# Performance work log

Hardware: AMD Instinct MI355X
Metric: run time of the kernel (lower is better)

## Reference

```python
import jax, jax.numpy as jnp
import numpy as np

B, T, H, V = 32, 16, 768, 32000
EPS = 1e-5


def _conv(x, w, stride, pad):
    return jax.lax.conv_general_dilated(
        x, w, (stride, stride), [(pad, pad), (pad, pad)],
        dimension_numbers=('NCHW', 'OIHW', 'NCHW'))


def _bn(x, g, b, m, v):
    inv = g / jnp.sqrt(v + EPS)
    return x * inv[None, :, None, None] + (b - m * inv)[None, :, None, None]


def setup_inputs() -> dict:
    key = jax.random.key(0)
    ks = iter(jax.random.split(key, 48))

    def rn(shape, s=0.02):
        return s * jax.random.normal(next(ks), shape, jnp.float32)

    def bn_params(c):
        g = 1.0 + 0.1 * jax.random.normal(next(ks), (c,), jnp.float32)
        b = 0.1 * jax.random.normal(next(ks), (c,), jnp.float32)
        m = 0.1 * jax.random.normal(next(ks), (c,), jnp.float32)
        v = jax.random.uniform(next(ks), (c,), jnp.float32, 0.5, 1.5)
        return g, b, m, v

    inp = {}
    inp['images'] = jax.random.normal(next(ks), (B, 3, 224, 224), jnp.float32)
    inp['captions'] = jax.random.randint(next(ks), (B, T), 0, V)

    inp['conv1_w'] = rn((64, 3, 7, 7))
    inp['bn1_g'], inp['bn1_b'], inp['bn1_m'], inp['bn1_v'] = bn_params(64)
    inp['conv2_w'] = rn((128, 64, 3, 3))
    inp['bn2_g'], inp['bn2_b'], inp['bn2_m'], inp['bn2_v'] = bn_params(128)
    inp['conv3_w'] = rn((256, 128, 3, 3))
    inp['bn3_g'], inp['bn3_b'], inp['bn3_m'], inp['bn3_v'] = bn_params(256)
    inp['conv4_w'] = rn((H, 256, 3, 3))
    inp['bn4_g'], inp['bn4_b'], inp['bn4_m'], inp['bn4_v'] = bn_params(H)

    emb = rn((V, H), 1.0)
    inp['emb_table'] = emb.at[0].set(0.0)  # padding_idx=0 row is zero
    inp['attn_w'] = rn((H, H))             # attn_proj (no bias)
    inp['w_ih'] = rn((4 * H, 2 * H))       # LSTM input weights (i,f,g,o)
    inp['w_hh'] = rn((4 * H, H))
    inp['b_ih'] = rn((4 * H,))
    inp['b_hh'] = rn((4 * H,))
    inp['fc_w'] = rn((V, H))
    inp['fc_b'] = rn((V,))
    return inp


def _forward(images, captions, conv1_w, bn1_g, bn1_b, bn1_m, bn1_v,
             conv2_w, bn2_g, bn2_b, bn2_m, bn2_v,
             conv3_w, bn3_g, bn3_b, bn3_m, bn3_v,
             conv4_w, bn4_g, bn4_b, bn4_m, bn4_v,
             emb_table, attn_w, w_ih, w_hh, b_ih, b_hh, fc_w, fc_b):
    # ---- ResNetEncoder ----
    x = jax.nn.relu(_bn(_conv(images, conv1_w, 2, 3), bn1_g, bn1_b, bn1_m, bn1_v))
    x = jax.lax.reduce_window(x, -jnp.inf, jax.lax.max, (1, 1, 3, 3), (1, 1, 2, 2),
                              ((0, 0), (0, 0), (1, 1), (1, 1)))
    x = jax.nn.relu(_bn(_conv(x, conv2_w, 1, 1), bn2_g, bn2_b, bn2_m, bn2_v))
    x = jax.nn.relu(_bn(_conv(x, conv3_w, 2, 1), bn3_g, bn3_b, bn3_m, bn3_v))
    x = jax.nn.relu(_bn(_conv(x, conv4_w, 1, 1), bn4_g, bn4_b, bn4_m, bn4_v))
    b, c, hh, ww = x.shape
    memory = x.reshape(b, c, hh * ww).transpose(0, 2, 1)[:, :196, :]  # [B,196,H]

    # ---- LSTMAttnDecoder ----
    emb = emb_table[captions]  # [B,T,H]
    h0 = jnp.zeros((b, H), jnp.float32)
    c0 = jnp.zeros((b, H), jnp.float32)

    def step(carry, e_t):
        h, cst = carry
        q = h @ attn_w.T                                    # [B,H]
        scores = jnp.einsum('bh,bmh->bm', q, memory)        # [B,196]
        ctx = jnp.einsum('bm,bmh->bh', jax.nn.softmax(scores, axis=-1), memory)
        xin = jnp.concatenate([e_t, ctx], axis=-1)          # [B,2H]
        gates = xin @ w_ih.T + b_ih + h @ w_hh.T + b_hh     # [B,4H]
        i, f, g, o = jnp.split(gates, 4, axis=-1)
        c_new = jax.nn.sigmoid(f) * cst + jax.nn.sigmoid(i) * jnp.tanh(g)
        h_new = jax.nn.sigmoid(o) * jnp.tanh(c_new)
        logits = h_new @ fc_w.T + fc_b                      # [B,V]
        return (h_new, c_new), logits

    (hT, cT), logits = jax.lax.scan(step, (h0, c0), emb.transpose(1, 0, 2))
    logits = logits.transpose(1, 0, 2)  # [B,T,V]
    return logits, (hT[None], cT[None])


def reference(images, captions, conv1_w, bn1_g, bn1_b, bn1_m, bn1_v,
              conv2_w, bn2_g, bn2_b, bn2_m, bn2_v,
              conv3_w, bn3_g, bn3_b, bn3_m, bn3_v,
              conv4_w, bn4_g, bn4_b, bn4_m, bn4_v,
              emb_table, attn_w, w_ih, w_hh, b_ih, b_hh, fc_w, fc_b):
    return _forward(images, captions, conv1_w, bn1_g, bn1_b, bn1_m, bn1_v,
                    conv2_w, bn2_g, bn2_b, bn2_m, bn2_v,
                    conv3_w, bn3_g, bn3_b, bn3_m, bn3_v,
                    conv4_w, bn4_g, bn4_b, bn4_m, bn4_v,
                    emb_table, attn_w, w_ih, w_hh, b_ih, b_hh, fc_w, fc_b)
```

## Files before the change

kernel.cpp:

```cpp
#include <hip/hip_runtime.h>
#include <math.h>

#define NB 32
#define NT 16
#define NH 768
#define NV 32000

typedef short bf16x8 __attribute__((ext_vector_type(8)));
typedef float floatx4 __attribute__((ext_vector_type(4)));
typedef unsigned short ushort_t;

__device__ __forceinline__ float bf2f(unsigned short h) {
    unsigned u = ((unsigned)h) << 16;
    return __builtin_bit_cast(float, u);
}
__device__ __forceinline__ unsigned short f2bf(float f) {
    unsigned u = __builtin_bit_cast(unsigned, f);
    u += 0x7fffu + ((u >> 16) & 1u);
    return (unsigned short)(u >> 16);
}
__device__ __forceinline__ float sigmoidf_(float x) { return 1.f / (1.f + expf(-x)); }

__device__ __forceinline__ int swz8(int bid, int N) {
    return (bid & 7) * (N >> 3) + (bid >> 3);
}

__device__ __forceinline__ bf16x8 cvt8(float4 a, float4 b) {
    bf16x8 t;
    t[0] = (short)f2bf(a.x); t[1] = (short)f2bf(a.y);
    t[2] = (short)f2bf(a.z); t[3] = (short)f2bf(a.w);
    t[4] = (short)f2bf(b.x); t[5] = (short)f2bf(b.y);
    t[6] = (short)f2bf(b.z); t[7] = (short)f2bf(b.w);
    return t;
}

#define SEG0 1216
#define SEG1 (SEG0 + 10240)
#define SEG2 (SEG1 + 73728)
#define SEG3 (SEG2 + 294912)
#define SEG4 (SEG3 + 1769472)
#define SEG5 (SEG4 + 589824)
#define SEG6 (SEG5 + 4718592)
#define SEG7 (SEG6 + 294912)
#define SEG8 (SEG7 + 393216)
#define SEG9 (SEG8 + 49152)
__global__ __launch_bounds__(256) void prep_all(
    const float* __restrict__ g1, const float* __restrict__ b1, const float* __restrict__ m1, const float* __restrict__ v1,
    const float* __restrict__ g2, const float* __restrict__ b2, const float* __restrict__ m2, const float* __restrict__ v2,
    const float* __restrict__ g3, const float* __restrict__ b3, const float* __restrict__ m3, const float* __restrict__ v3,
    const float* __restrict__ g4, const float* __restrict__ b4, const float* __restrict__ m4, const float* __restrict__ v4,
    float* __restrict__ s1, float* __restrict__ o1, float* __restrict__ s2, float* __restrict__ o2,
    float* __restrict__ s3, float* __restrict__ o3, float* __restrict__ s4, float* __restrict__ o4,
    const float* __restrict__ conv1_w, ushort_t* __restrict__ wb1,
    const float* __restrict__ conv2_w, ushort_t* __restrict__ wb2,
    const float* __restrict__ conv3_w, ushort_t* __restrict__ wb3,
    const float* __restrict__ conv4_w, ushort_t* __restrict__ wb4,
    const float* __restrict__ attn_w, ushort_t* __restrict__ wattnTP,
    const float* __restrict__ w_ih, const float* __restrict__ w_hh, ushort_t* __restrict__ wcombP,
    ushort_t* __restrict__ wihL,
    const int* __restrict__ caps, const float* __restrict__ table, ushort_t* __restrict__ e512P,
    float* __restrict__ hbuf, float* __restrict__ cbuf, ushort_t* __restrict__ xinA,
    unsigned long long* __restrict__ halo, long long n8) {
    long long gi = (long long)blockIdx.x * 256 + threadIdx.x;
    if (gi < SEG0) {
        int i = (int)gi;
        const float *g, *b, *m, *v;
        float *s, *o;
        int c;
        if (i < 64)        { g = g1; b = b1; m = m1; v = v1; s = s1; o = o1; c = i; }
        else if (i < 192)  { g = g2; b = b2; m = m2; v = v2; s = s2; o = o2; c = i - 64; }
        else if (i < 448)  { g = g3; b = b3; m = m3; v = v3; s = s3; o = o3; c = i - 192; }
        else               { g = g4; b = b4; m = m4; v = v4; s = s4; o = o4; c = i - 448; }
        float inv = g[c] * rsqrtf(v[c] + 1e-5f);
        s[c] = inv;
        o[c] = b[c] - m[c] * inv;
    } else if (gi < SEG1) {
        int idx = (int)(gi - SEG0);
        int co = idx / 160, k = idx % 160;
        wb1[idx] = (k < 147) ? f2bf(conv1_w[co * 147 + k]) : (ushort_t)0;
    } else if (gi < SEG4) {
        const float* w;
        ushort_t* dst;
        int CIN, idx;
        if (gi < SEG2)      { w = conv2_w; dst = wb2; CIN = 64;  idx = (int)(gi - SEG1); }
        else if (gi < SEG3) { w = conv3_w; dst = wb3; CIN = 128; idx = (int)(gi - SEG2); }
        else                { w = conv4_w; dst = wb4; CIN = 256; idx = (int)(gi - SEG3); }
        int e = idx & 7, lane = (idx >> 3) & 63, j = (idx >> 9) & 3;
        int r = idx >> 11;
        int KQ = CIN >> 5;
        int kq = r % KQ; r /= KQ;
        int tap = r % 9; int nt = r / 9;
        int co = nt * 64 + j * 16 + (lane & 15);
        int ci = kq * 32 + (lane >> 4) * 8 + e;
        dst[idx] = f2bf(w[((size_t)co * CIN + ci) * 9 + tap]);
    } else if (gi < SEG5) {
        int idx = (int)(gi - SEG4);
        int e = idx & 7, lane = (idx >> 3) & 63, j = (idx >> 9) & 3;
        int t = idx >> 11;
        int kq = t % 24, nt = t / 24;
        int n = nt * 64 + 16 * j + (lane & 15);
        int k = kq * 32 + (lane >> 4) * 8 + e;
        wattnTP[idx] = f2bf(attn_w[(size_t)k * 768 + n]);
    } else if (gi < SEG6) {
        int idx = (int)(gi - SEG5);
        int e = idx & 7, lane = (idx >> 3) & 63;
        int t = idx >> 9;
        int kq = t % 48, gg = t / 48;
        int g = gg & 3, bx = gg >> 2;
        int j = g * 768 + bx * 16 + (lane & 15);
        int k = kq * 32 + (lane >> 4) * 8 + e;
        float v = (k < NH) ? w_ih[(size_t)j * (2 * NH) + NH + k] : w_hh[(size_t)j * NH + (k - NH)];
        wcombP[idx] = f2bf(v);
    } else if (gi < SEG7) {
        int idx = (int)(gi - SEG6);
        int r = idx / 96, g = idx % 96;
        const float4* s = (const float4*)(w_ih + (size_t)r * 1536 + g * 8);
        *(bf16x8*)(wihL + (size_t)idx * 8) = cvt8(s[0], s[1]);
    } else if (gi < SEG8) {
        int idx = (int)(gi - SEG7);
        int e = idx & 7, lane = (idx >> 3) & 63, i = (idx >> 9) & 3;
        int t2 = idx >> 11;
        int kq = t2 % 24, mt = t2 / 24;
        int r = mt * 64 + i * 16 + (lane & 15);
        int k = kq * 32 + (lane >> 4) * 8 + e;
        int t = r >> 5, b = r & 31;
        e512P[idx] = f2bf(table[(size_t)caps[b * NT + t] * NH + k]);
    } else if (gi < SEG9) {
        int i = (int)(gi - SEG8);
        xinA[i] = 0;
        if (i < NB * NH) { hbuf[i] = 0.f; cbuf[i] = 0.f; }
    } else {
        long long j = gi - SEG9;
        if (j < n8) halo[j] = 0ULL;
    }
}

__global__ __launch_bounds__(256) void im2col1(const float* __restrict__ img, ushort_t* __restrict__ A) {
    int idx = blockIdx.x * 256 + threadIdx.x;
    const int total = 121856 * 160;
    if (idx >= total) return;
    int k = idx % 160;
    int m = idx / 160;
    ushort_t v = 0;
    if (k < 147) {
        int b = m / 3808;
        int rm = m % 3808;
        int y = rm / 112, x = rm % 112;
        int ci = k / 49;
        int r = k % 49;
        int ky = r / 7, kx = r % 7;
        int iy = 2 * y - 3 + ky;
        int ix = 2 * x - 3 + kx;
        if ((unsigned)iy < 224u && (unsigned)ix < 224u)
            v = f2bf(img[((size_t)(b * 3 + ci) * 224 + iy) * 224 + ix]);
    }
    A[idx] = v;
}

__global__ __launch_bounds__(256) void cvt_b16rows(const float* __restrict__ src, ushort_t* __restrict__ dst,
                                                   int cols8, int ldsrc, int total8) {
    int i = blockIdx.x * 256 + threadIdx.x;
    if (i >= total8) return;
    int r = i / cols8, g = i % cols8;
    const float4* s = (const float4*)(src + (size_t)r * ldsrc + g * 8);
    *(bf16x8*)(dst + (size_t)i * 8) = cvt8(s[0], s[1]);
}

__global__ __launch_bounds__(256) void conv1_gemm(
    const ushort_t* __restrict__ A, const ushort_t* __restrict__ Bw,
    const float* __restrict__ scale, const float* __restrict__ bias,
    ushort_t* __restrict__ out) {
    int lane = threadIdx.x & 63, w = threadIdx.x >> 6;
    int m0 = (blockIdx.x * 4 + w) * 64;
    int lr = lane & 15, kl = (lane >> 4) * 8;
    floatx4 acc[4][4];
    #pragma unroll
    for (int i = 0; i < 4; ++i)
        #pragma unroll
        for (int j = 0; j < 4; ++j) acc[i][j] = 0.f;
    #pragma unroll
    for (int k0 = 0; k0 < 160; k0 += 32) {
        bf16x8 a[4], bb[4];
        #pragma unroll
        for (int i = 0; i < 4; ++i) a[i] = *(const bf16x8*)(A + (size_t)(m0 + 16 * i + lr) * 160 + kl + k0);
        #pragma unroll
        for (int j = 0; j < 4; ++j) bb[j] = *(const bf16x8*)(Bw + (size_t)(16 * j + lr) * 160 + kl + k0);
        #pragma unroll
        for (int i = 0; i < 4; ++i)
            #pragma unroll
            for (int j = 0; j < 4; ++j)
                acc[i][j] = __builtin_amdgcn_mfma_f32_16x16x32_bf16(a[i], bb[j], acc[i][j], 0, 0, 0);
    }
    #pragma unroll
    for (int i = 0; i < 4; ++i) {
        #pragma unroll
        for (int r = 0; r < 4; ++r) {
            int m = m0 + 16 * i + (lane >> 4) * 4 + r;
            int b = m / 3808;
            int rm = m % 3808;
            int y = rm / 112, x = rm % 112;
            #pragma unroll
            for (int j = 0; j < 4; ++j) {
                int n = 16 * j + lr;
                float v = fmaxf(acc[i][j][r] * scale[n] + bias[n], 0.f);
                out[((size_t)(b * 34 + y) * 112 + x) * 64 + n] = f2bf(v);
            }
        }
    }
}

__global__ __launch_bounds__(256) void pool_kernel(const ushort_t* __restrict__ in,
                                                   ushort_t* __restrict__ hal2) {
    int idx = blockIdx.x * 256 + threadIdx.x;
    const int total = 32 * 17 * 56 * 8;
    if (idx >= total) return;
    int c8 = idx & 7;
    int rest = idx >> 3;
    int x = rest % 56; rest /= 56;
    int y = rest % 17; int b = rest / 17;
    float mx[8];
    #pragma unroll
    for (int j = 0; j < 8; ++j) mx[j] = -INFINITY;
    for (int dy = -1; dy <= 1; ++dy) {
        int iy = 2 * y + dy;
        if ((unsigned)iy >= 34u) continue;
        for (int dx = -1; dx <= 1; ++dx) {
            int ix = 2 * x + dx;
            if ((unsigned)ix >= 112u) continue;
            bf16x8 v = *(const bf16x8*)(in + (((size_t)(b * 34 + iy)) * 112 + ix) * 64 + c8 * 8);
            #pragma unroll
            for (int j = 0; j < 8; ++j) mx[j] = fmaxf(mx[j], bf2f((unsigned short)v[j]));
        }
    }
    bf16x8 o;
    #pragma unroll
    for (int j = 0; j < 8; ++j) o[j] = (short)f2bf(mx[j]);
    *(bf16x8*)(hal2 + (((size_t)(b * 19 + y + 1)) * 58 + (x + 1)) * 64 + c8 * 8) = o;
}

template <int CIN, int HH, int WH, int STRIDE, int HOUT, int WOUT, int COUT, int OH, int OW>
__global__ __launch_bounds__(64) void conv_mfma(
    const ushort_t* __restrict__ in, const ushort_t* __restrict__ wtP,
    const float* __restrict__ scale, const float* __restrict__ bias,
    ushort_t* __restrict__ out) {
    const int KQ = CIN / 32;
    const int NK = 9 * KQ;
    const int MT = (32 * HOUT * WOUT) / 64;
    const int NTL = COUT / 64;
    int id = swz8(blockIdx.x, MT * NTL);
    int mt = id % MT, nt = id / MT;
    int lane = threadIdx.x;
    int lr = lane & 15, kl = (lane >> 4) * 8;
    int rowoff[4];
    #pragma unroll
    for (int i = 0; i < 4; ++i) {
        int m = mt * 64 + 16 * i + lr;
        int b = m / (HOUT * WOUT);
        int rm = m % (HOUT * WOUT);
        int y = rm / WOUT, x = rm % WOUT;
        rowoff[i] = ((b * HH + y * STRIDE) * WH + x * STRIDE) * CIN + kl;
    }
    floatx4 acc[4][4];
    #pragma unroll
    for (int i = 0; i < 4; ++i)
        #pragma unroll
        for (int j = 0; j < 4; ++j) acc[i][j] = 0.f;

    auto ioffOf = [&](int ks) {
        int tap = ks / KQ;
        int k0 = (ks & (KQ - 1)) * 32;
        int ky = tap / 3, kx = tap - ky * 3;
        return (ky * WH + kx) * CIN + k0;
    };
    const ushort_t* bbase = wtP + ((size_t)nt * 9 * KQ * 4 * 64 + lane) * 8;

    bf16x8 aC[4], bC[4], aN[4], bN[4];
    {
        int io = ioffOf(0);
        #pragma unroll
        for (int i = 0; i < 4; ++i) aC[i] = *(const bf16x8*)(in + rowoff[i] + io);
        #pragma unroll
        for (int j = 0; j < 4; ++j) bC[j] = *(const bf16x8*)(bbase + ((size_t)j * 64) * 8);
    }
    for (int ks = 0; ks < NK; ks += 2) {
        {
            int io = ioffOf(ks + 1);
            #pragma unroll
            for (int i = 0; i < 4; ++i) aN[i] = *(const bf16x8*)(in + rowoff[i] + io);
            #pragma unroll
            for (int j = 0; j < 4; ++j) bN[j] = *(const bf16x8*)(bbase + ((size_t)((ks + 1) * 4 + j) * 64) * 8);
        }
        #pragma unroll
        for (int i = 0; i < 4; ++i)
            #pragma unroll
            for (int j = 0; j < 4; ++j)
                acc[i][j] = __builtin_amdgcn_mfma_f32_16x16x32_bf16(aC[i], bC[j], acc[i][j], 0, 0, 0);
        if (ks + 2 < NK) {
            int io = ioffOf(ks + 2);
            #pragma unroll
            for (int i = 0; i < 4; ++i) aC[i] = *(const bf16x8*)(in + rowoff[i] + io);
            #pragma unroll
            for (int j = 0; j < 4; ++j) bC[j] = *(const bf16x8*)(bbase + ((size_t)((ks + 2) * 4 + j) * 64) * 8);
        }
        #pragma unroll
        for (int i = 0; i < 4; ++i)
            #pragma unroll
            for (int j = 0; j < 4; ++j)
                acc[i][j] = __builtin_amdgcn_mfma_f32_16x16x32_bf16(aN[i], bN[j], acc[i][j], 0, 0, 0);
    }
    #pragma unroll
    for (int i = 0; i < 4; ++i) {
        #pragma unroll
        for (int r = 0; r < 4; ++r) {
            int m = mt * 64 + 16 * i + (lane >> 4) * 4 + r;
            int b = m / (HOUT * WOUT);
            int rm = m % (HOUT * WOUT);
            int y = rm / WOUT, x = rm % WOUT;
            #pragma unroll
            for (int j = 0; j < 4; ++j) {
                int n = nt * 64 + 16 * j + lr;
                float v = fmaxf(acc[i][j][r] * scale[n] + bias[n], 0.f);
                out[((size_t)(b * OH + y + 1) * OW + (x + 1)) * COUT + n] = f2bf(v);
            }
        }
    }
}

__global__ __launch_bounds__(256) void conv4_lds(
    const ushort_t* __restrict__ in, const ushort_t* __restrict__ wtP,
    const float* __restrict__ scale, const float* __restrict__ bias,
    ushort_t* __restrict__ memv) {
    const int CIN = 256, WH = 30;
    __shared__ ushort_t at[2][4 * 64 * 40];
    int tid = threadIdx.x;
    int lane = tid & 63, w = tid >> 6;
    int mt = blockIdx.x;
    int nt = blockIdx.y * 4 + w;
    int lr = lane & 15, kl = (lane >> 4) * 8;
    int srow = tid >> 2, sc = tid & 3;
    int m_s = mt * 64 + srow;
    int b_s = m_s / 196, rm_s = m_s % 196;
    int y_s = rm_s / 28, x_s = rm_s % 28;
    const ushort_t* arow = in + ((size_t)(b_s * 10 + y_s) * 30 + x_s) * CIN + sc * 8;
    int woff = srow * 40 + sc * 8;

    floatx4 acc[4][4];
    #pragma unroll
    for (int i = 0; i < 4; ++i)
        #pragma unroll
        for (int j = 0; j < 4; ++j) acc[i][j] = 0.f;

    auto ioffOf = [&](int ks) {
        int tap = ks >> 3;
        int k0 = (ks & 7) * 32;
        int ky = tap / 3, kx = tap - ky * 3;
        return (ky * WH + kx) * CIN + k0;
    };
    const ushort_t* bbase = wtP + ((size_t)nt * 72 * 4 * 64 + lane) * 8;

    bf16x8 st[4];
    #pragma unroll
    for (int j = 0; j < 4; ++j) st[j] = *(const bf16x8*)(arow + ioffOf(j));
    for (int p = 0; p < 18; ++p) {
        ushort_t* buf = &at[p & 1][0];
        #pragma unroll
        for (int j = 0; j < 4; ++j)
            *(bf16x8*)(buf + j * 2560 + woff) = st[j];
        if (p < 17) {
            #pragma unroll
            for (int j = 0; j < 4; ++j)
                st[j] = *(const bf16x8*)(arow + ioffOf((p + 1) * 4 + j));
        }
        __syncthreads();
        #pragma unroll
        for (int kk = 0; kk < 4; ++kk) {
            int ks = p * 4 + kk;
            bf16x8 a[4], bb[4];
            #pragma unroll
            for (int j = 0; j < 4; ++j)
                bb[j] = *(const bf16x8*)(bbase + ((size_t)(ks * 4 + j) * 64) * 8);
            #pragma unroll
            for (int i = 0; i < 4; ++i)
                a[i] = *(const bf16x8*)(buf + kk * 2560 + (16 * i + lr) * 40 + kl);
            #pragma unroll
            for (int i = 0; i < 4; ++i)
                #pragma unroll
                for (int j = 0; j < 4; ++j)
                    acc[i][j] = __builtin_amdgcn_mfma_f32_16x16x32_bf16(a[i], bb[j], acc[i][j], 0, 0, 0);
        }
        __syncthreads();
    }
    #pragma unroll
    for (int i = 0; i < 4; ++i) {
        #pragma unroll
        for (int r = 0; r < 4; ++r) {
            int m = mt * 64 + 16 * i + (lane >> 4) * 4 + r;
            #pragma unroll
            for (int j = 0; j < 4; ++j) {
                int n = nt * 64 + 16 * j + lr;
                float v = fmaxf(acc[i][j][r] * scale[n] + bias[n], 0.f);
                memv[(size_t)m * 768 + n] = f2bf(v);
            }
        }
    }
}

__global__ __launch_bounds__(256) void kmat_lds(
    const ushort_t* __restrict__ memv, const ushort_t* __restrict__ Bp,
    ushort_t* __restrict__ KT) {
    __shared__ ushort_t at[2][4 * 64 * 40];
    int tid = threadIdx.x;
    int lane = tid & 63, w = tid >> 6;
    int mt = blockIdx.x;
    int nt = blockIdx.y * 4 + w;
    int lr = lane & 15, kl = (lane >> 4) * 8;
    int srow = tid >> 2, sc = tid & 3;
    const ushort_t* arow = memv + (size_t)(mt * 64 + srow) * 768 + sc * 8;
    int woff = srow * 40 + sc * 8;
    const ushort_t* bbase = Bp + ((size_t)nt * 24 * 4 * 64 + lane) * 8;

    floatx4 acc[4][4];
    #pragma unroll
    for (int i = 0; i < 4; ++i)
        #pragma unroll
        for (int j = 0; j < 4; ++j) acc[i][j] = 0.f;

    bf16x8 st[4];
    #pragma unroll
    for (int j = 0; j < 4; ++j) st[j] = *(const bf16x8*)(arow + j * 32);
    for (int p = 0; p < 6; ++p) {
        ushort_t* buf = &at[p & 1][0];
        #pragma unroll
        for (int j = 0; j < 4; ++j)
            *(bf16x8*)(buf + j * 2560 + woff) = st[j];
        if (p < 5) {
            #pragma unroll
            for (int j = 0; j < 4; ++j)
                st[j] = *(const bf16x8*)(arow + ((p + 1) * 4 + j) * 32);
        }
        __syncthreads();
        #pragma unroll
        for (int kk = 0; kk < 4; ++kk) {
            int ks = p * 4 + kk;
            bf16x8 a[4], bb[4];
            #pragma unroll
            for (int j = 0; j < 4; ++j)
                bb[j] = *(const bf16x8*)(bbase + ((size_t)(ks * 4 + j) * 64) * 8);
            #pragma unroll
            for (int i = 0; i < 4; ++i)
                a[i] = *(const bf16x8*)(buf + kk * 2560 + (16 * i + lr) * 40 + kl);
            #pragma unroll
            for (int i = 0; i < 4; ++i)
                #pragma unroll
                for (int j = 0; j < 4; ++j)
                    acc[i][j] = __builtin_amdgcn_mfma_f32_16x16x32_bf16(a[i], bb[j], acc[i][j], 0, 0, 0);
        }
        __syncthreads();
    }
    #pragma unroll
    for (int i = 0; i < 4; ++i) {
        #pragma unroll
        for (int r = 0; r < 4; ++r) {
            int mg = mt * 64 + 16 * i + (lane >> 4) * 4 + r;
            int b = mg / 196, m = mg % 196;
            #pragma unroll
            for (int j = 0; j < 4; ++j) {
                int n = nt * 64 + 16 * j + lr;
                KT[(((size_t)b * 96 + (n >> 3)) * 196 + m) * 8 + (n & 7)] = f2bf(acc[i][j][r]);
            }
        }
    }
}

template <int REMAP>
__global__ __launch_bounds__(256, 4) void gemm_ldsb(
    const ushort_t* __restrict__ Ap, const ushort_t* __restrict__ Bb,
    const float* __restrict__ bias1, const float* __restrict__ bias2,
    float* __restrict__ C, int N) {
    __shared__ ushort_t bt[2][64 * 72];
    int tid = threadIdx.x;
    int lane = tid & 63, w = tid >> 6;
    int nblk = (N >> 6) * 2;
    int id = swz8(blockIdx.x, nblk);
    int nt = id >> 1, mh = id & 1;
    int n0 = nt * 64;
    int mt = mh * 4 + w;
    int lr = lane & 15, hi = lane >> 4;
    int srow = tid >> 2, sc = tid & 3;
    const ushort_t* gsrc = Bb + (size_t)(n0 + srow) * 768 + sc * 8;
    int woff = srow * 72 + sc * 8;
    floatx4 acc[4][4];
    #pragma unroll
    for (int i = 0; i < 4; ++i)
        #pragma unroll
        for (int j = 0; j < 4; ++j) acc[i][j] = 0.f;
    bf16x8 s0 = *(const bf16x8*)(gsrc);
    bf16x8 s1 = *(const bf16x8*)(gsrc + 32);
    for (int kc = 0; kc < 12; ++kc) {
        ushort_t* bufw = &bt[kc & 1][0];
        *(bf16x8*)(bufw + woff) = s0;
        *(bf16x8*)(bufw + woff + 32) = s1;
        if (kc < 11) {
            const ushort_t* p = gsrc + (size_t)(kc + 1) * 64;
            s0 = *(const bf16x8*)(p);
            s1 = *(const bf16x8*)(p + 32);
        }
        __syncthreads();
        const ushort_t* bufr = &bt[kc & 1][0];
        #pragma unroll
        for (int kk = 0; kk < 2; ++kk) {
            int kq = kc * 2 + kk;
            bf16x8 bfr[4], a[4];
            #pragma unroll
            for (int j = 0; j < 4; ++j)
                bfr[j] = *(const bf16x8*)(bufr + (j * 16 + lr) * 72 + kk * 32 + hi * 8);
            #pragma unroll
            for (int i = 0; i < 4; ++i)
                a[i] = *(const bf16x8*)(Ap + ((((size_t)mt * 24 + kq) * 4 + i) * 64 + lane) * 8);
            #pragma unroll
            for (int i = 0; i < 4; ++i)
                #pragma unroll
                for (int j = 0; j < 4; ++j)
                    acc[i][j] = __builtin_amdgcn_mfma_f32_16x16x32_bf16(a[i], bfr[j], acc[i][j], 0, 0, 0);
        }
    }
    #pragma unroll
    for (int i = 0; i < 4; ++i) {
        #pragma unroll
        for (int rr = 0; rr < 4; ++rr) {
            int m = mt * 64 + 16 * i + hi * 4 + rr;
            #pragma unroll
            for (int j = 0; j < 4; ++j) {
                int n = n0 + 16 * j + lr;
                float vv = acc[i][j][rr];
                if (bias1) vv += bias1[n];
                if (bias2) vv += bias2[n];
                if (REMAP) {
                    int t = m >> 5, b = m & 31;
                    C[(size_t)((b << 4) + t) * NV + n] = vv;
                } else {
                    C[(size_t)m * N + n] = vv;
                }
            }
        }
    }
}

__global__ __launch_bounds__(768) void attn2(
    ushort_t* __restrict__ xin, const ushort_t* __restrict__ KT,
    const ushort_t* __restrict__ mem) {
    __shared__ float hq[NH];
    __shared__ float sl[196];
    __shared__ float red[16];
    int b = blockIdx.x, halfb = blockIdx.y, tid = threadIdx.x;
    hq[tid] = bf2f(xin[(size_t)b * 1536 + NH + tid]);
    __syncthreads();
    if (tid < 392) {
        int m = tid >> 1, half = tid & 1;
        const ushort_t* basep = KT + (((size_t)b * 96 + half * 48) * 196 + m) * 8;
        float acc = 0.f;
        #pragma unroll 4
        for (int k8 = 0; k8 < 48; ++k8) {
            bf16x8 v = *(const bf16x8*)(basep + (size_t)k8 * 196 * 8);
            const float* qp = hq + (half * 48 + k8) * 8;
            #pragma unroll
            for (int j = 0; j < 8; ++j)
                acc = fmaf(bf2f((unsigned short)v[j]), qp[j], acc);
        }
        acc += __shfl_xor(acc, 1);
        if (!half) sl[m] = acc;
    }
    __syncthreads();
    float sc = (tid < 196) ? sl[tid] : -INFINITY;
    float v = sc;
    #pragma unroll
    for (int off = 32; off; off >>= 1) v = fmaxf(v, __shfl_down(v, off));
    if ((tid & 63) == 0) red[tid >> 6] = v;
    __syncthreads();
    if (tid == 0) {
        float m = red[0];
        for (int i = 1; i < 12; ++i) m = fmaxf(m, red[i]);
        red[12] = m;
    }
    __syncthreads();
    float mx = red[12];
    float e = (tid < 196) ? expf(sc - mx) : 0.f;
    __syncthreads();
    v = e;
    #pragma unroll
    for (int off = 32; off; off >>= 1) v += __shfl_down(v, off);
    if ((tid & 63) == 0) red[tid >> 6] = v;
    __syncthreads();
    if (tid == 0) {
        float s = red[0];
        for (int i = 1; i < 12; ++i) s += red[i];
        red[12] = 1.f / s;
    }
    __syncthreads();
    if (tid < 196) sl[tid] = e * red[12];
    __syncthreads();
    if (tid < 384) {
        int d = halfb * 384 + tid;
        float acc = 0.f;
        const ushort_t* mb = mem + (size_t)b * 196 * NH + d;
        #pragma unroll 4
        for (int m = 0; m < 196; ++m) acc = fmaf(sl[m], bf2f(mb[(size_t)m * NH]), acc);
        xin[(size_t)b * 1536 + d] = f2bf(acc);
    }
}

__global__ __launch_bounds__(256) void step_fused(
    const ushort_t* __restrict__ xin_r, const ushort_t* __restrict__ wcombP,
    const float* __restrict__ eg_t,
    float* __restrict__ cbuf, float* __restrict__ hbuf,
    ushort_t* __restrict__ xin_w, ushort_t* __restrict__ hallP, int tstep) {
    __shared__ float pbuf[4][64][33];
    int lane = threadIdx.x & 63, w = threadIdx.x >> 6;
    int bx = blockIdx.x;
    int lr = lane & 15, kl = (lane >> 4) * 8;
    floatx4 acc[2][4];
    #pragma unroll
    for (int i = 0; i < 2; ++i)
        #pragma unroll
        for (int g = 0; g < 4; ++g) acc[i][g] = 0.f;
    for (int kq = 0; kq < 12; ++kq) {
        int k = w * 384 + kq * 32;
        bf16x8 a[2], bb[4];
        #pragma unroll
        for (int i = 0; i < 2; ++i)
            a[i] = *(const bf16x8*)(xin_r + (size_t)(16 * i + lr) * 1536 + k + kl);
        #pragma unroll
        for (int g = 0; g < 4; ++g)
            bb[g] = *(const bf16x8*)(wcombP + (((size_t)(bx * 4 + g) * 48 + (w * 12 + kq)) * 64 + lane) * 8);
        #pragma unroll
        for (int i = 0; i < 2; ++i)
            #pragma unroll
            for (int g = 0; g < 4; ++g)
                acc[i][g] = __builtin_amdgcn_mfma_f32_16x16x32_bf16(a[i], bb[g], acc[i][g], 0, 0, 0);
    }
    #pragma unroll
    for (int i = 0; i < 2; ++i)
        #pragma unroll
        for (int g = 0; g < 4; ++g)
            #pragma unroll
            for (int r = 0; r < 4; ++r) {
                int m = 16 * i + (lane >> 4) * 4 + r;
                pbuf[w][g * 16 + lr][m] = acc[i][g][r];
            }
    __syncthreads();
    int tid = threadIdx.x;
    #pragma unroll
    for (int o = 0; o < 2; ++o) {
        int pid = tid * 2 + o;
        int m = pid & 31, c = pid >> 5;
        int kcol = bx * 16 + c;
        float gi = 0.f, gf = 0.f, gg = 0.f, go = 0.f;
        #pragma unroll
        for (int ww = 0; ww < 4; ++ww) {
            gi += pbuf[ww][c][m];
            gf += pbuf[ww][16 + c][m];
            gg += pbuf[ww][32 + c][m];
            go += pbuf[ww][48 + c][m];
        }
        const float* eg = eg_t + (size_t)m * 3072;
        gi += eg[kcol];
        gf += eg[768 + kcol];
        gg += eg[1536 + kcol];
        go += eg[2304 + kcol];
        float cst = cbuf[m * 768 + kcol];
        float cn = sigmoidf_(gf) * cst + sigmoidf_(gi) * tanhf(gg);
        float hn = sigmoidf_(go) * tanhf(cn);
        cbuf[m * 768 + kcol] = cn;
        hbuf[m * 768 + kcol] = hn;
        ushort_t hb = f2bf(hn);
        xin_w[(size_t)m * 1536 + NH + kcol] = hb;
        int rrow = tstep * 32 + m;
        int mtp = rrow >> 6, ip = (rrow >> 4) & 3, lrp = rrow & 15;
        int kqp = kcol >> 5, hip = (kcol >> 3) & 3, ep = kcol & 7;
        hallP[((((size_t)mtp * 24 + kqp) * 4 + ip) * 64 + (lrp | (hip << 4))) * 8 + ep] = hb;
    }
}

__global__ __launch_bounds__(256) void copy_hc(const float* __restrict__ h, const float* __restrict__ c,
                                               float* __restrict__ out) {
    int i = blockIdx.x * 256 + threadIdx.x;
    if (i < NB * NH) {
        out[(size_t)NB * NT * NV + i] = h[i];
        out[(size_t)NB * NT * NV + NB * NH + i] = c[i];
    }
}

extern "C" void kernel_launch(void* const* d_in, const int* in_sizes, int n_in,
                              void* d_out, int out_size, void* d_ws, size_t ws_size,
                              hipStream_t stream) {
    const float* images   = (const float*)d_in[0];
    const int*   captions = (const int*)d_in[1];
    const float* conv1_w  = (const float*)d_in[2];
    const float* bn1_g = (const float*)d_in[3], *bn1_b = (const float*)d_in[4];
    const float* bn1_m = (const float*)d_in[5], *bn1_v = (const float*)d_in[6];
    const float* conv2_w  = (const float*)d_in[7];
    const float* bn2_g = (const float*)d_in[8], *bn2_b = (const float*)d_in[9];
    const float* bn2_m = (const float*)d_in[10], *bn2_v = (const float*)d_in[11];
    const float* conv3_w  = (const float*)d_in[12];
    const float* bn3_g = (const float*)d_in[13], *bn3_b = (const float*)d_in[14];
    const float* bn3_m = (const float*)d_in[15], *bn3_v = (const float*)d_in[16];
    const float* conv4_w  = (const float*)d_in[17];
    const float* bn4_g = (const float*)d_in[18], *bn4_b = (const float*)d_in[19];
    const float* bn4_m = (const float*)d_in[20], *bn4_v = (const float*)d_in[21];
    const float* emb_table = (const float*)d_in[22];
    const float* attn_w   = (const float*)d_in[23];
    const float* w_ih     = (const float*)d_in[24];
    const float* w_hh     = (const float*)d_in[25];
    const float* b_ih     = (const float*)d_in[26];
    const float* b_hh     = (const float*)d_in[27];
    const float* fc_w     = (const float*)d_in[28];
    const float* fc_b     = (const float*)d_in[29];
    float* out = (float*)d_out;

    char* base = (char*)d_ws;
    size_t off = 0;
    auto alloc = [&](size_t bytes) { char* p = base + off; off += (bytes + 255) & ~(size_t)255; return p; };
    float* s1 = (float*)alloc(64 * 4);   float* bb1 = (float*)alloc(64 * 4);
    float* s2 = (float*)alloc(128 * 4);  float* bb2 = (float*)alloc(128 * 4);
    float* s3 = (float*)alloc(256 * 4);  float* bb3 = (float*)alloc(256 * 4);
    float* s4 = (float*)alloc(768 * 4);  float* bb4 = (float*)alloc(768 * 4);
    ushort_t* c1out = (ushort_t*)alloc((size_t)32 * 34 * 112 * 64 * 2);
    size_t halo_start = off;
    ushort_t* hal2 = (ushort_t*)alloc((size_t)32 * 19 * 58 * 64 * 2);
    ushort_t* hal3 = (ushort_t*)alloc((size_t)32 * 18 * 58 * 128 * 2);
    ushort_t* hal4 = (ushort_t*)alloc((size_t)32 * 10 * 30 * 256 * 2);
    size_t halo_bytes = off - halo_start;
    ushort_t* memv = (ushort_t*)alloc((size_t)32 * 196 * 768 * 2);
    ushort_t* KT   = (ushort_t*)alloc((size_t)32 * 96 * 196 * 8 * 2);
    ushort_t* wb1 = (ushort_t*)alloc((size_t)64 * 160 * 2);
    ushort_t* wb2 = (ushort_t*)alloc((size_t)128 * 9 * 64 * 2);
    ushort_t* wb3 = (ushort_t*)alloc((size_t)256 * 9 * 128 * 2);
    ushort_t* wb4 = (ushort_t*)alloc((size_t)768 * 9 * 256 * 2);
    ushort_t* wattnTP = (ushort_t*)alloc((size_t)768 * 768 * 2);
    ushort_t* wcombP = (ushort_t*)alloc((size_t)3072 * 1536 * 2);
    ushort_t* wihL = (ushort_t*)alloc((size_t)3072 * 768 * 2);
    ushort_t* e512P = (ushort_t*)alloc((size_t)512 * 768 * 2);
    float* eg   = (float*)alloc((size_t)512 * 3072 * 4);
    ushort_t* HallP = (ushort_t*)alloc((size_t)512 * 768 * 2);
    float* hbuf = (float*)alloc(NB * NH * 4);
    float* cbuf = (float*)alloc(NB * NH * 4);
    ushort_t* xinA = (ushort_t*)alloc((size_t)NB * 1536 * 2);
    ushort_t* xinB = (ushort_t*)alloc((size_t)NB * 1536 * 2);
    char* ubig = alloc((size_t)NV * NH * 2);
    ushort_t* imcol = (ushort_t*)ubig;
    ushort_t* fcwb  = (ushort_t*)ubig;

    long long n8 = (long long)(halo_bytes / 8);
    long long prep_total = (long long)SEG9 + n8;
    prep_all<<<(unsigned)((prep_total + 255) / 256), 256, 0, stream>>>(
        bn1_g, bn1_b, bn1_m, bn1_v, bn2_g, bn2_b, bn2_m, bn2_v,
        bn3_g, bn3_b, bn3_m, bn3_v, bn4_g, bn4_b, bn4_m, bn4_v,
        s1, bb1, s2, bb2, s3, bb3, s4, bb4,
        conv1_w, wb1, conv2_w, wb2, conv3_w, wb3, conv4_w, wb4,
        attn_w, wattnTP, w_ih, w_hh, wcombP, wihL,
        captions, emb_table, e512P,
        hbuf, cbuf, xinA,
        (unsigned long long*)hal2, n8);

    gemm_ldsb<0><<<96, 256, 0, stream>>>(e512P, wihL, b_ih, b_hh, eg, 3072);

    im2col1<<<(121856 * 160 + 255) / 256, 256, 0, stream>>>(images, imcol);
    conv1_gemm<<<476, 256, 0, stream>>>(imcol, wb1, s1, bb1, c1out);
    cvt_b16rows<<<(NV * 96 + 255) / 256, 256, 0, stream>>>(fc_w, fcwb, 96, 768, NV * 96);
    pool_kernel<<<(32 * 17 * 56 * 8 + 255) / 256, 256, 0, stream>>>(c1out, hal2);
    conv_mfma<64, 19, 58, 1, 16, 56, 128, 18, 58>
        <<<896, 64, 0, stream>>>(hal2, wb2, s2, bb2, hal3);
    conv_mfma<128, 18, 58, 2, 8, 28, 256, 10, 30>
        <<<448, 64, 0, stream>>>(hal3, wb3, s3, bb3, hal4);
    conv4_lds<<<dim3(98, 3), 256, 0, stream>>>(hal4, wb4, s4, bb4, memv);

    kmat_lds<<<dim3(98, 3), 256, 0, stream>>>(memv, wattnTP, KT);

    ushort_t* xcur = xinA;
    ushort_t* xnxt = xinB;
    for (int t = 0; t < NT; ++t) {
        attn2<<<dim3(NB, 2), NH, 0, stream>>>(xcur, KT, memv);
        step_fused<<<48, 256, 0, stream>>>(
            xcur, wcombP, eg + (size_t)t * NB * 3072, cbuf, hbuf, xnxt, HallP, t);
        ushort_t* tmp = xcur; xcur = xnxt; xnxt = tmp;
    }

    gemm_ldsb<1><<<1000, 256, 0, stream>>>(HallP, fcwb, fc_b, nullptr, out, NV);

    copy_hc<<<(NB * NH + 255) / 256, 256, 0, stream>>>(hbuf, cbuf, out);
}
```

Measured before the change: 851.6 us.

## Share im2col A tiles across output-channel waves in LDS for conv2/conv3

Replaces the single-wave conv_mfma kernels for conv2 and conv3 with multi-wave blocks. Each block stages the A (im2col) tile into double-buffered LDS once, and the waves covering different output-channel tiles all read it, so activation loads are no longer repeated from global memory per channel tile. It also folds the final h/c copy into block 0 of the final FC GEMM, removing one kernel launch. The cost is extra __syncthreads per stage and fewer, larger blocks (112 for conv3), which may lower occupancy and parallelism.

```diff
diff --git a/kernel.cpp b/kernel.cpp
--- a/kernel.cpp
+++ b/kernel.cpp
@@ -238,28 +238,24 @@
     *(bf16x8*)(hal2 + (((size_t)(b * 19 + y + 1)) * 58 + (x + 1)) * 64 + c8 * 8) = o;
 }
 
-template <int CIN, int HH, int WH, int STRIDE, int HOUT, int WOUT, int COUT, int OH, int OW>
-__global__ __launch_bounds__(64) void conv_mfma(
+__global__ __launch_bounds__(128) void conv2_lds(
     const ushort_t* __restrict__ in, const ushort_t* __restrict__ wtP,
     const float* __restrict__ scale, const float* __restrict__ bias,
     ushort_t* __restrict__ out) {
-    const int KQ = CIN / 32;
-    const int NK = 9 * KQ;
-    const int MT = (32 * HOUT * WOUT) / 64;
-    const int NTL = COUT / 64;
-    int id = swz8(blockIdx.x, MT * NTL);
-    int mt = id % MT, nt = id / MT;
-    int lane = threadIdx.x;
+    const int CIN = 64, WH = 58;
+    __shared__ ushort_t at[2][3 * 2560];
+    int tid = threadIdx.x;
+    int lane = tid & 63, w = tid >> 6;
+    int mt = swz8(blockIdx.x, 448);
+    int nt = w;
     int lr = lane & 15, kl = (lane >> 4) * 8;
-    int rowoff[4];
-    #pragma unroll
-    for (int i = 0; i < 4; ++i) {
-        int m = mt * 64 + 16 * i + lr;
-        int b = m / (HOUT * WOUT);
-        int rm = m % (HOUT * WOUT);
-        int y = rm / WOUT, x = rm % WOUT;
-        rowoff[i] = ((b * HH + y * STRIDE) * WH + x * STRIDE) * CIN + kl;
-    }
+    int srow = tid >> 1, sc = tid & 1;
+    int m_s = mt * 64 + srow;
+    int b_s = m_s / 896, rm_s = m_s % 896;
+    int y_s = rm_s / 56, x_s = rm_s % 56;
+    const ushort_t* arow = in + ((size_t)(b_s * 19 + y_s) * 58 + x_s) * CIN + sc * 16;
+    int woff = srow * 40 + sc * 16;
+
     floatx4 acc[4][4];
     #pragma unroll
     for (int i = 0; i < 4; ++i)
@@ -267,60 +263,147 @@
         for (int j = 0; j < 4; ++j) acc[i][j] = 0.f;
 
     auto ioffOf = [&](int ks) {
-        int tap = ks / KQ;
-        int k0 = (ks & (KQ - 1)) * 32;
+        int tap = ks >> 1;
+        int k0 = (ks & 1) * 32;
         int ky = tap / 3, kx = tap - ky * 3;
         return (ky * WH + kx) * CIN + k0;
     };
-    const ushort_t* bbase = wtP + ((size_t)nt * 9 * KQ * 4 * 64 + lane) * 8;
-
-    bf16x8 aC[4], bC[4], aN[4], bN[4];
-    {
-        int io = ioffOf(0);
-        #pragma unroll
-        for (int i = 0; i < 4; ++i) aC[i] = *(const bf16x8*)(in + rowoff[i] + io);
-        #pragma unroll
-        for (int j = 0; j < 4; ++j) bC[j] = *(const bf16x8*)(bbase + ((size_t)j * 64) * 8);
-    }
-    for (int ks = 0; ks < NK; ks += 2) {
-        {
-            int io = ioffOf(ks + 1);
-            #pragma unroll
-            for (int i = 0; i < 4; ++i) aN[i] = *(const bf16x8*)(in + rowoff[i] + io);
-            #pragma unroll
-            for (int j = 0; j < 4; ++j) bN[j] = *(const bf16x8*)(bbase + ((size_t)((ks + 1) * 4 + j) * 64) * 8);
-        }
-        #pragma unroll
-        for (int i = 0; i < 4; ++i)
+    const ushort_t* bbase = wtP + ((size_t)nt * 18 * 4 * 64 + lane) * 8;
+
+    bf16x8 st[3][2];
+    #pragma unroll
+    for (int j = 0; j < 3; ++j) {
+        int io = ioffOf(j);
+        st[j][0] = *(const bf16x8*)(arow + io);
+        st[j][1] = *(const bf16x8*)(arow + io + 8);
+    }
+    for (int p = 0; p < 6; ++p) {
+        ushort_t* buf = &at[p & 1][0];
+        #pragma unroll
+        for (int j = 0; j < 3; ++j) {
+            *(bf16x8*)(buf + j * 2560 + woff) = st[j][0];
+            *(bf16x8*)(buf + j * 2560 + woff + 8) = st[j][1];
+        }
+        if (p < 5) {
+            #pragma unroll
+            for (int j = 0; j < 3; ++j) {
+                int io = ioffOf((p + 1) * 3 + j);
+                st[j][0] = *(const bf16x8*)(arow + io);
+                st[j][1] = *(const bf16x8*)(arow + io + 8);
+            }
+        }
+        __syncthreads();
+        #pragma unroll
+        for (int kk = 0; kk < 3; ++kk) {
+            int ks = p * 3 + kk;
+            bf16x8 a[4], bb[4];
             #pragma unroll
             for (int j = 0; j < 4; ++j)
-                acc[i][j] = __builtin_amdgcn_mfma_f32_16x16x32_bf16(aC[i], bC[j], acc[i][j], 0, 0, 0);
-        if (ks + 2 < NK) {
-            int io = ioffOf(ks + 2);
-            #pragma unroll
-            for (int i = 0; i < 4; ++i) aC[i] = *(const bf16x8*)(in + rowoff[i] + io);
-            #pragma unroll
-            for (int j = 0; j < 4; ++j) bC[j] = *(const bf16x8*)(bbase + ((size_t)((ks + 2) * 4 + j) * 64) * 8);
-        }
-        #pragma unroll
-        for (int i = 0; i < 4; ++i)
-            #pragma unroll
-            for (int j = 0; j < 4; ++j)
-                acc[i][j] = __builtin_amdgcn_mfma_f32_16x16x32_bf16(aN[i], bN[j], acc[i][j], 0, 0, 0);
+                bb[j] = *(const bf16x8*)(bbase + ((size_t)(ks * 4 + j) * 64) * 8);
+            #pragma unroll
+            for (int i = 0; i < 4; ++i)
+                a[i] = *(const bf16x8*)(buf + kk * 2560 + (16 * i + lr) * 40 + kl);
+            #pragma unroll
+            for (int i = 0; i < 4; ++i)
+                #pragma unroll
+                for (int j = 0; j < 4; ++j)
+                    acc[i][j] = __builtin_amdgcn_mfma_f32_16x16x32_bf16(a[i], bb[j], acc[i][j], 0, 0, 0);
+        }
+        __syncthreads();
     }
     #pragma unroll
     for (int i = 0; i < 4; ++i) {
         #pragma unroll
         for (int r = 0; r < 4; ++r) {
             int m = mt * 64 + 16 * i + (lane >> 4) * 4 + r;
-            int b = m / (HOUT * WOUT);
-            int rm = m % (HOUT * WOUT);
-            int y = rm / WOUT, x = rm % WOUT;
+            int b = m / 896, rm = m % 896;
+            int y = rm / 56, x = rm % 56;
             #pragma unroll
             for (int j = 0; j < 4; ++j) {
                 int n = nt * 64 + 16 * j + lr;
                 float v = fmaxf(acc[i][j][r] * scale[n] + bias[n], 0.f);
-                out[((size_t)(b * OH + y + 1) * OW + (x + 1)) * COUT + n] = f2bf(v);
+                out[((size_t)(b * 18 + y + 1) * 58 + (x + 1)) * 128 + n] = f2bf(v);
+            }
+        }
+    }
+}
+
+__global__ __launch_bounds__(256) void conv3_lds(
+    const ushort_t* __restrict__ in, const ushort_t* __restrict__ wtP,
+    const float* __restrict__ scale, const float* __restrict__ bias,
+    ushort_t* __restrict__ out) {
+    const int CIN = 128, WH = 58;
+    __shared__ ushort_t at[2][4 * 2560];
+    int tid = threadIdx.x;
+    int lane = tid & 63, w = tid >> 6;
+    int mt = swz8(blockIdx.x, 112);
+    int nt = w;
+    int lr = lane & 15, kl = (lane >> 4) * 8;
+    int srow = tid >> 2, sc = tid & 3;
+    int m_s = mt * 64 + srow;
+    int b_s = m_s / 224, rm_s = m_s % 224;
+    int y_s = rm_s / 28, x_s = rm_s % 28;
+    const ushort_t* arow = in + ((size_t)(b_s * 18 + y_s * 2) * 58 + x_s * 2) * CIN + sc * 8;
+    int woff = srow * 40 + sc * 8;
+
+    floatx4 acc[4][4];
+    #pragma unroll
+    for (int i = 0; i < 4; ++i)
+        #pragma unroll
+        for (int j = 0; j < 4; ++j) acc[i][j] = 0.f;
+
+    auto ioffOf = [&](int ks) {
+        int tap = ks >> 2;
+        int k0 = (ks & 3) * 32;
+        int ky = tap / 3, kx = tap - ky * 3;
+        return (ky * WH + kx) * CIN + k0;
+    };
+    const ushort_t* bbase = wtP + ((size_t)nt * 36 * 4 * 64 + lane) * 8;
+
+    bf16x8 st[4];
+    #pragma unroll
+    for (int j = 0; j < 4; ++j) st[j] = *(const bf16x8*)(arow + ioffOf(j));
+    for (int p = 0; p < 9; ++p) {
+        ushort_t* buf = &at[p & 1][0];
+        #pragma unroll
+        for (int j = 0; j < 4; ++j)
+            *(bf16x8*)(buf + j * 2560 + woff) = st[j];
+        if (p < 8) {
+            #pragma unroll
+            for (int j = 0; j < 4; ++j)
+                st[j] = *(const bf16x8*)(arow + ioffOf((p + 1) * 4 + j));
+        }
+        __syncthreads();
+        #pragma unroll
+        for (int kk = 0; kk < 4; ++kk) {
+            int ks = p * 4 + kk;
+            bf16x8 a[4], bb[4];
+            #pragma unroll
+            for (int j = 0; j < 4; ++j)
+                bb[j] = *(const bf16x8*)(bbase + ((size_t)(ks * 4 + j) * 64) * 8);
+            #pragma unroll
+            for (int i = 0; i < 4; ++i)
+                a[i] = *(const bf16x8*)(buf + kk * 2560 + (16 * i + lr) * 40 + kl);
+            #pragma unroll
+            for (int i = 0; i < 4; ++i)
+                #pragma unroll
+                for (int j = 0; j < 4; ++j)
+                    acc[i][j] = __builtin_amdgcn_mfma_f32_16x16x32_bf16(a[i], bb[j], acc[i][j], 0, 0, 0);
+        }
+        __syncthreads();
+    }
+    #pragma unroll
+    for (int i = 0; i < 4; ++i) {
+        #pragma unroll
+        for (int r = 0; r < 4; ++r) {
+            int m = mt * 64 + 16 * i + (lane >> 4) * 4 + r;
+            int b = m / 224, rm = m % 224;
+            int y = rm / 28, x = rm % 28;
+            #pragma unroll
+            for (int j = 0; j < 4; ++j) {
+                int n = nt * 64 + 16 * j + lr;
+                float v = fmaxf(acc[i][j][r] * scale[n] + bias[n], 0.f);
+                out[((size_t)(b * 10 + y + 1) * 30 + (x + 1)) * 256 + n] = f2bf(v);
             }
         }
     }
@@ -476,7 +559,8 @@
 __global__ __launch_bounds__(256, 4) void gemm_ldsb(
     const ushort_t* __restrict__ Ap, const ushort_t* __restrict__ Bb,
     const float* __restrict__ bias1, const float* __restrict__ bias2,
-    float* __restrict__ C, int N) {
+    float* __restrict__ C, int N,
+    const float* __restrict__ hcp, const float* __restrict__ ccp) {
     __shared__ ushort_t bt[2][64 * 72];
     int tid = threadIdx.x;
     int lane = tid & 63, w = tid >> 6;
@@ -542,6 +626,12 @@
                     C[(size_t)m * N + n] = vv;
                 }
             }
+        }
+    }
+    if (REMAP && blockIdx.x == 0) {
+        for (int i = tid; i < NB * NH; i += 256) {
+            C[(size_t)NB * NT * NV + i] = hcp[i];
+            C[(size_t)NB * NT * NV + NB * NH + i] = ccp[i];
         }
     }
 }
@@ -678,15 +768,6 @@
         int mtp = rrow >> 6, ip = (rrow >> 4) & 3, lrp = rrow & 15;
         int kqp = kcol >> 5, hip = (kcol >> 3) & 3, ep = kcol & 7;
         hallP[((((size_t)mtp * 24 + kqp) * 4 + ip) * 64 + (lrp | (hip << 4))) * 8 + ep] = hb;
-    }
-}
-
-__global__ __launch_bounds__(256) void copy_hc(const float* __restrict__ h, const float* __restrict__ c,
-                                               float* __restrict__ out) {
-    int i = blockIdx.x * 256 + threadIdx.x;
-    if (i < NB * NH) {
-        out[(size_t)NB * NT * NV + i] = h[i];
-        out[(size_t)NB * NT * NV + NB * NH + i] = c[i];
     }
 }
 
@@ -762,16 +843,14 @@
         hbuf, cbuf, xinA,
         (unsigned long long*)hal2, n8);
 
-    gemm_ldsb<0><<<96, 256, 0, stream>>>(e512P, wihL, b_ih, b_hh, eg, 3072);
+    gemm_ldsb<0><<<96, 256, 0, stream>>>(e512P, wihL, b_ih, b_hh, eg, 3072, nullptr, nullptr);
 
     im2col1<<<(121856 * 160 + 255) / 256, 256, 0, stream>>>(images, imcol);
     conv1_gemm<<<476, 256, 0, stream>>>(imcol, wb1, s1, bb1, c1out);
     cvt_b16rows<<<(NV * 96 + 255) / 256, 256, 0, stream>>>(fc_w, fcwb, 96, 768, NV * 96);
     pool_kernel<<<(32 * 17 * 56 * 8 + 255) / 256, 256, 0, stream>>>(c1out, hal2);
-    conv_mfma<64, 19, 58, 1, 16, 56, 128, 18, 58>
-        <<<896, 64, 0, stream>>>(hal2, wb2, s2, bb2, hal3);
-    conv_mfma<128, 18, 58, 2, 8, 28, 256, 10, 30>
-        <<<448, 64, 0, stream>>>(hal3, wb3, s3, bb3, hal4);
+    conv2_lds<<<448, 128, 0, stream>>>(hal2, wb2, s2, bb2, hal3);
+    conv3_lds<<<112, 256, 0, stream>>>(hal3, wb3, s3, bb3, hal4);
     conv4_lds<<<dim3(98, 3), 256, 0, stream>>>(hal4, wb4, s4, bb4, memv);
 
     kmat_lds<<<dim3(98, 3), 256, 0, stream>>>(memv, wattnTP, KT);
@@ -785,7 +864,5 @@
         ushort_t* tmp = xcur; xcur = xnxt; xnxt = tmp;
     }
 
-    gemm_ldsb<1><<<1000, 256, 0, stream>>>(HallP, fcwb, fc_b, nullptr, out, NV);
-
-    copy_hc<<<(NB * NH + 255) / 256, 256, 0, stream>>>(hbuf, cbuf, out);
-}
+    gemm_ldsb<1><<<1000, 256, 0, stream>>>(HallP, fcwb, fc_b, nullptr, out, NV, hbuf, cbuf);
+}
```

After: 855.1 us. About the same (+0.4%).
